# Kernel optimization log

Hardware: AMD Instinct MI355X
Metric: run time of the kernel (lower is better)

Reference implementation:

```python
import jax, jax.numpy as jnp
import numpy as np

B, S, I, H, O = 64, 512, 256, 1024, 128

def setup_inputs() -> dict:
    key = jax.random.key(0)
    ks = jax.random.split(key, 9)
    s_in = 1.0 / np.sqrt(I)
    s_h = 1.0 / np.sqrt(H)
    return {
        "x": jax.random.normal(ks[0], (B, S, I), dtype=jnp.float32),
        "W_in": jax.random.uniform(ks[1], (H, I), jnp.float32, -s_in, s_in),
        "b_in": jax.random.uniform(ks[2], (H,), jnp.float32, -s_in, s_in),
        "W_rec": jax.random.uniform(ks[3], (H, H), jnp.float32, -s_h, s_h),
        "b_rec": jax.random.uniform(ks[4], (H,), jnp.float32, -s_h, s_h),
        "tau_m": jnp.full((H,), 2.0, dtype=jnp.float32),
        "tau_n": jnp.full((H,), 2.0, dtype=jnp.float32),
        "W_out": jax.random.uniform(ks[5], (O, H), jnp.float32, -s_h, s_h),
        "b_out": jax.random.uniform(ks[6], (O,), jnp.float32, -s_h, s_h),
    }

def reference(x, W_in, b_in, W_rec, b_rec, tau_m, tau_n, W_out, b_out):
    b, s, _ = x.shape
    h = W_in.shape[0]
    alpha = jax.nn.sigmoid(tau_m)  # [H]
    beta = jax.nn.sigmoid(tau_n)   # [H]
    # Precompute feedforward GEMM for all timesteps at once: [B,S,H]
    ff = jnp.einsum('bsi,hi->bsh', x, W_in) + b_in

    def step(carry, ff_t):
        mem, d, prev_spike = carry  # each [B,H]
        total = ff_t + prev_spike @ W_rec.T + b_rec
        d = beta * d + (1.0 - beta) * total
        mem = alpha * mem + (1.0 - alpha) * d
        spike = (mem > 1.0).astype(mem.dtype)
        mem = mem * (1.0 - spike)
        out = jax.nn.sigmoid(spike @ W_out.T + b_out)  # [B,O]
        return (mem, d, spike), out

    zeros = jnp.zeros((b, h), dtype=x.dtype)
    _, outs = jax.lax.scan(step, (zeros, zeros, zeros), jnp.swapaxes(ff, 0, 1))
    return jnp.swapaxes(outs, 0, 1)  # [B,S,O]
```

## Files before the change

kernel.cpp:

```cpp
#include <hip/hip_runtime.h>
#include <hip/hip_bf16.h>
#include <stdint.h>

#define B_ 64
#define S_ 512
#define I_ 256
#define H_ 1024
#define O_ 128
#define M_ (B_*S_)

typedef float f32x4 __attribute__((ext_vector_type(4)));
typedef unsigned short u16x4 __attribute__((ext_vector_type(4)));
typedef unsigned short u16x8 __attribute__((ext_vector_type(8)));

__device__ __forceinline__ unsigned short f2bf(float f) {
    unsigned u = __float_as_uint(f);
    u += 0x7FFFu + ((u >> 16) & 1u);
    return (unsigned short)(u >> 16);
}
__device__ __forceinline__ float bf2f(unsigned short s) {
    return __uint_as_float((unsigned)s << 16);
}

__global__ void __launch_bounds__(256) k0_convert(
    const float* __restrict__ x, const float* __restrict__ Win,
    uint8_t* __restrict__ xf8, uint8_t* __restrict__ wf8,
    unsigned* __restrict__ firstCross)
{
    __shared__ unsigned lds32[64 * 65];
    const int i = blockIdx.x;
    const int t = threadIdx.x;

    const float* src;
    uint8_t* dstBase;
    int kqStride;
    if (i < 512) {
        const int r0 = i * 64;
        src = x + (size_t)r0 * 256;
        const int T = i >> 1;
        const int rbase = (i & 1) * 4;
        dstBase = xf8 + (size_t)T * 32768 + rbase * 512;
        kqStride = 4096;
    } else {
        const int i2 = i - 512;
        src = Win + (size_t)(i2 * 64) * 256;
        dstBase = wf8 + (size_t)i2 * 16384;
        kqStride = 2048;
    }

#pragma unroll
    for (int j = 0; j < 16; ++j) {
        const int f = j * 256 + t;
        const int lrow = f >> 6, c4 = f & 63;
        float4 v = *(const float4*)(src + (size_t)lrow * 256 + c4 * 4);
        int w0 = 0;
        w0 = __builtin_amdgcn_cvt_pk_fp8_f32(v.x, v.y, w0, false);
        w0 = __builtin_amdgcn_cvt_pk_fp8_f32(v.z, v.w, w0, true);
        lds32[lrow * 65 + c4] = (unsigned)w0;
    }
    __syncthreads();

#pragma unroll
    for (int j = 0; j < 4; ++j) {
        const int c = j * 256 + t;
        const int kq  = c >> 7;
        const int rem = c & 127;
        const int rbl = rem >> 5;
        const int l0  = (rem & 31) * 2;
        const int r   = l0 & 15;
        const int q   = l0 >> 4;
        const int lrow = rbl * 16 + r;
        const int c0 = kq * 8 + q * 2;
        uint4 o;
        o.x = lds32[lrow * 65 + c0];
        o.y = lds32[lrow * 65 + c0 + 1];
        o.z = lds32[(lrow + 1) * 65 + c0];
        o.w = lds32[(lrow + 1) * 65 + c0 + 1];
        *(uint4*)(dstBase + kq * kqStride + rbl * 512 + l0 * 8) = o;
    }

    if (i == 0 && t < 64) firstCross[t] = 0xFFFFFFFFu;
}

__global__ void __launch_bounds__(256, 4) kf_gemm_scan(
    const uint8_t* __restrict__ xf8, const uint8_t* __restrict__ wf8,
    const float* __restrict__ b_in, const float* __restrict__ b_rec,
    const float* __restrict__ tau_m, const float* __restrict__ tau_n,
    unsigned* __restrict__ firstCross)
{
    __shared__ uint8_t lsbuf[16384];

    const int tid  = threadIdx.x;
    const int w    = tid >> 6;
    const int lane = tid & 63;
    const int idx  = blockIdx.x;
    const int b    = (idx & 7) | ((idx >> 7) << 3);
    const int hn   = (idx >> 3) & 15;
    const int colrow = lane & 15;
    const int quad   = lane >> 4;

    float alpha = 0.f, beta = 0.f, cbr = 0.f, oma = 0.f, ombr = 0.f;
    float d = 0.f, mem = 0.f;
    unsigned cross = 0xFFFFFFFFu;
    if (tid < 64) {
        const int hs = hn * 64 + tid;
        alpha = 1.f / (1.f + expf(-tau_m[hs]));
        beta  = 1.f / (1.f + expf(-tau_n[hs]));
        oma = 1.f - alpha; ombr = 1.f - beta;
        cbr = ombr * (b_in[hs] + b_rec[hs]);
    }

    const uint8_t* wB = wf8 + (size_t)hn * 16384 + lane * 8;
    long long bq[32];
#pragma unroll
    for (int kq = 0; kq < 8; ++kq)
#pragma unroll
        for (int ni = 0; ni < 4; ++ni)
            bq[kq * 4 + ni] = *(const long long*)(wB + kq * 2048 + ni * 512);

    for (int tt = 0; tt < 4; ++tt) {
        const uint8_t* xA = xf8 + (size_t)(b * 4 + tt) * 32768
                          + w * 1024 + lane * 8;

        f32x4 acc[2][4];
#pragma unroll
        for (int mi = 0; mi < 2; ++mi)
#pragma unroll
            for (int ni = 0; ni < 4; ++ni)
                acc[mi][ni] = (f32x4){0.f, 0.f, 0.f, 0.f};

#pragma unroll
        for (int kq = 0; kq < 8; ++kq) {
            long long a[2];
#pragma unroll
            for (int mi = 0; mi < 2; ++mi)
                a[mi] = *(const long long*)(xA + kq * 4096 + mi * 512);
#pragma unroll
            for (int mi = 0; mi < 2; ++mi)
#pragma unroll
                for (int ni = 0; ni < 4; ++ni)
                    acc[mi][ni] = __builtin_amdgcn_mfma_f32_16x16x32_fp8_fp8(
                        a[mi], bq[kq * 4 + ni], acc[mi][ni], 0, 0, 0);
        }

        __syncthreads();

#pragma unroll
        for (int mi = 0; mi < 2; ++mi) {
            const int t0 = w * 32 + mi * 16 + quad * 4;
            const int gb = (t0 >> 3) * 1024 + (t0 & 7) * 2;
#pragma unroll
            for (int ni = 0; ni < 4; ++ni) {
                const int h0 = ni * 16 + colrow;
                u16x4 p;
                p[0] = f2bf(acc[mi][ni][0]);
                p[1] = f2bf(acc[mi][ni][1]);
                p[2] = f2bf(acc[mi][ni][2]);
                p[3] = f2bf(acc[mi][ni][3]);
                *(u16x4*)(lsbuf + gb + h0 * 16) = p;
            }
        }
        __syncthreads();

        if (tid < 64) {
            const uint8_t* rowp = lsbuf + tid * 16;
            for (int tl0 = 0; tl0 < 128; tl0 += 16) {
                const int gb = (tl0 >> 3) * 1024;
                u16x8 v0 = *(const u16x8*)(rowp + gb);
                u16x8 v1 = *(const u16x8*)(rowp + gb + 1024);
                float f[16];
#pragma unroll
                for (int u = 0; u < 8; ++u) { f[u] = bf2f(v0[u]); f[8 + u] = bf2f(v1[u]); }
#pragma unroll
                for (int u = 0; u < 16; ++u) {
                    d   = fmaf(beta,  d,   fmaf(ombr, f[u], cbr));
                    mem = fmaf(alpha, mem, oma * d);
                    if (mem > 1.0f) {
                        unsigned ts = (unsigned)(tt * 128 + tl0 + u);
                        if (ts < cross) cross = ts;
                    }
                }
            }
        }
    }

    if (tid < 64 && cross != 0xFFFFFFFFu) atomicMin(firstCross + b, cross);
}

__global__ void __launch_bounds__(1024) k3_repair(
    const float* __restrict__ x, const float* __restrict__ W_in,
    const float* __restrict__ b_in,
    const float* __restrict__ W_rec, const float* __restrict__ b_rec,
    const float* __restrict__ tau_m, const float* __restrict__ tau_n,
    const float* __restrict__ W_out, const float* __restrict__ b_out,
    const unsigned* __restrict__ firstCross,
    unsigned long long* __restrict__ gmask,
    float* __restrict__ out)
{
    const int b = blockIdx.x;
    if (firstCross[b] == 0xFFFFFFFFu) return;
    const int h = threadIdx.x;
    __shared__ float xrow[I_];
    __shared__ unsigned long long msk[16];
    if (h < 16) msk[h] = 0ull;
    const float alpha = 1.f / (1.f + expf(-tau_m[h]));
    const float beta  = 1.f / (1.f + expf(-tau_n[h]));
    const float bsum  = b_in[h] + b_rec[h];
    const float* wi = W_in + (size_t)h * I_;
    const float* wr = W_rec + (size_t)h * H_;
    float d = 0.f, mem = 0.f;
    for (int t = 0; t < S_; ++t) {
        __syncthreads();
        if (h < I_) xrow[h] = x[((size_t)b * S_ + t) * I_ + h];
        __syncthreads();
        float ffv = 0.f;
        for (int k = 0; k < I_; ++k) ffv += xrow[k] * wi[k];
        float rec = 0.f;
#pragma unroll
        for (int wd = 0; wd < 16; ++wd) {
            unsigned long long mw = msk[wd];
            while (mw) {
                int bit = __ffsll((long long)mw) - 1;
                rec += wr[(wd << 6) + bit];
                mw &= (mw - 1);
            }
        }
        float tot = ffv + bsum + rec;
        d   = beta  * d   + (1.f - beta)  * tot;
        mem = alpha * mem + (1.f - alpha) * d;
        int sp = (mem > 1.0f) ? 1 : 0;
        if (sp) mem = 0.f;
        unsigned long long bal = __ballot(sp);
        __syncthreads();
        if ((h & 63) == 0) {
            msk[h >> 6] = bal;
            gmask[((size_t)b * S_ + t) * 16 + (h >> 6)] = bal;
        }
    }
    __syncthreads();
    __threadfence_block();
    for (int i = h; i < S_ * O_; i += 1024) {
        const int t = i >> 7, o = i & (O_ - 1);
        float logit = b_out[o];
        const unsigned long long* m = gmask + ((size_t)b * S_ + t) * 16;
        const float* wo = W_out + (size_t)o * H_;
        for (int wd = 0; wd < 16; ++wd) {
            unsigned long long mw = m[wd];
            while (mw) {
                int bit = __ffsll((long long)mw) - 1;
                logit += wo[(wd << 6) + bit];
                mw &= (mw - 1);
            }
        }
        out[((size_t)b * S_ + t) * O_ + o] = 1.f / (1.f + expf(-logit));
    }
}

__global__ void __launch_bounds__(256) k4_out(
    const float* __restrict__ b_out,
    const unsigned* __restrict__ firstCross,
    float* __restrict__ out)
{
    const int i4 = blockIdx.x * 256 + threadIdx.x;
    const int b  = i4 >> 14;
    if (firstCross[b] != 0xFFFFFFFFu) return;
    const int o4 = i4 & 31;
    float4 v = *(const float4*)(b_out + o4 * 4);
    float4 r;
    r.x = 1.f / (1.f + expf(-v.x));
    r.y = 1.f / (1.f + expf(-v.y));
    r.z = 1.f / (1.f + expf(-v.z));
    r.w = 1.f / (1.f + expf(-v.w));
    *(float4*)(out + (size_t)i4 * 4) = r;
}

extern "C" void kernel_launch(void* const* d_in, const int* in_sizes, int n_in,
                              void* d_out, int out_size, void* d_ws, size_t ws_size,
                              hipStream_t stream) {
    const float* x     = (const float*)d_in[0];
    const float* W_in  = (const float*)d_in[1];
    const float* b_in  = (const float*)d_in[2];
    const float* W_rec = (const float*)d_in[3];
    const float* b_rec = (const float*)d_in[4];
    const float* tau_m = (const float*)d_in[5];
    const float* tau_n = (const float*)d_in[6];
    const float* W_out = (const float*)d_in[7];
    const float* b_out = (const float*)d_in[8];
    float* out = (float*)d_out;

    char* ws = (char*)d_ws;
    size_t off = 0;
    uint8_t* xf8 = (uint8_t*)(ws + off);               off += (size_t)M_ * I_;
    uint8_t* wf8 = (uint8_t*)(ws + off);               off += (size_t)H_ * I_;
    unsigned long long* gmask = (unsigned long long*)(ws + off); off += (size_t)B_ * S_ * 16 * 8;
    unsigned* firstCross = (unsigned*)(ws + off);      off += 256;
    if (ws_size < off) return;

    k0_convert<<<528, 256, 0, stream>>>(x, W_in, xf8, wf8, firstCross);
    kf_gemm_scan<<<1024, 256, 0, stream>>>(xf8, wf8, b_in, b_rec, tau_m, tau_n,
                                           firstCross);
    k3_repair<<<64, 1024, 0, stream>>>(x, W_in, b_in, W_rec, b_rec, tau_m, tau_n,
                                       W_out, b_out, firstCross, gmask, out);
    k4_out<<<4096, 256, 0, stream>>>(b_out, firstCross, out);
}
```

Baseline: 136.5 us.

## Warp-specialize GEMM-scan kernel with double-buffered LDS and halve convert block size

```diff
diff --git a/kernel.cpp b/kernel.cpp
--- a/kernel.cpp
+++ b/kernel.cpp
@@ -27,29 +27,26 @@
     uint8_t* __restrict__ xf8, uint8_t* __restrict__ wf8,
     unsigned* __restrict__ firstCross)
 {
-    __shared__ unsigned lds32[64 * 65];
+    __shared__ unsigned lds32[32 * 65];
     const int i = blockIdx.x;
     const int t = threadIdx.x;
 
     const float* src;
     uint8_t* dstBase;
     int kqStride;
-    if (i < 512) {
-        const int r0 = i * 64;
-        src = x + (size_t)r0 * 256;
-        const int T = i >> 1;
-        const int rbase = (i & 1) * 4;
-        dstBase = xf8 + (size_t)T * 32768 + rbase * 512;
+    if (i < 1024) {
+        src = x + (size_t)(i * 32) * 256;
+        dstBase = xf8 + (size_t)(i >> 2) * 32768 + (i & 3) * 2 * 512;
         kqStride = 4096;
     } else {
-        const int i2 = i - 512;
-        src = Win + (size_t)(i2 * 64) * 256;
-        dstBase = wf8 + (size_t)i2 * 16384;
+        const int i2 = i - 1024;
+        src = Win + (size_t)(i2 * 32) * 256;
+        dstBase = wf8 + (size_t)(i2 >> 1) * 16384 + (i2 & 1) * 2 * 512;
         kqStride = 2048;
     }
 
 #pragma unroll
-    for (int j = 0; j < 16; ++j) {
+    for (int j = 0; j < 8; ++j) {
         const int f = j * 256 + t;
         const int lrow = f >> 6, c4 = f & 63;
         float4 v = *(const float4*)(src + (size_t)lrow * 256 + c4 * 4);
@@ -61,12 +58,11 @@
     __syncthreads();
 
 #pragma unroll
-    for (int j = 0; j < 4; ++j) {
+    for (int j = 0; j < 2; ++j) {
         const int c = j * 256 + t;
-        const int kq  = c >> 7;
-        const int rem = c & 127;
-        const int rbl = rem >> 5;
-        const int l0  = (rem & 31) * 2;
+        const int kq  = c >> 6;
+        const int rbl = (c >> 5) & 1;
+        const int l0  = (c & 31) * 2;
         const int r   = l0 & 15;
         const int q   = l0 >> 4;
         const int lrow = rbl * 16 + r;
@@ -82,13 +78,14 @@
     if (i == 0 && t < 64) firstCross[t] = 0xFFFFFFFFu;
 }
 
-__global__ void __launch_bounds__(256, 4) kf_gemm_scan(
+__global__ void __launch_bounds__(320) kf_gemm_scan(
     const uint8_t* __restrict__ xf8, const uint8_t* __restrict__ wf8,
     const float* __restrict__ b_in, const float* __restrict__ b_rec,
     const float* __restrict__ tau_m, const float* __restrict__ tau_n,
     unsigned* __restrict__ firstCross)
 {
-    __shared__ uint8_t lsbuf[16384];
+    __shared__ uint8_t lB[16384];
+    __shared__ uint8_t lS[2][16384];
 
     const int tid  = threadIdx.x;
     const int w    = tid >> 6;
@@ -99,71 +96,76 @@
     const int colrow = lane & 15;
     const int quad   = lane >> 4;
 
+    if (w < 4) {
+        const uint8_t* gB = wf8 + (size_t)hn * 16384;
+#pragma unroll
+        for (int j = 0; j < 4; ++j) {
+            const int off = (w * 4 + j) * 1024 + lane * 16;
+            __builtin_amdgcn_global_load_lds(
+                (const __attribute__((address_space(1))) void*)(gB + off),
+                (__attribute__((address_space(3))) void*)(lB + off), 16, 0, 0);
+        }
+    }
+
     float alpha = 0.f, beta = 0.f, cbr = 0.f, oma = 0.f, ombr = 0.f;
     float d = 0.f, mem = 0.f;
     unsigned cross = 0xFFFFFFFFu;
-    if (tid < 64) {
-        const int hs = hn * 64 + tid;
+    if (w == 4) {
+        const int hs = hn * 64 + lane;
         alpha = 1.f / (1.f + expf(-tau_m[hs]));
         beta  = 1.f / (1.f + expf(-tau_n[hs]));
         oma = 1.f - alpha; ombr = 1.f - beta;
         cbr = ombr * (b_in[hs] + b_rec[hs]);
     }
-
-    const uint8_t* wB = wf8 + (size_t)hn * 16384 + lane * 8;
-    long long bq[32];
-#pragma unroll
-    for (int kq = 0; kq < 8; ++kq)
-#pragma unroll
-        for (int ni = 0; ni < 4; ++ni)
-            bq[kq * 4 + ni] = *(const long long*)(wB + kq * 2048 + ni * 512);
+    __syncthreads();
 
     for (int tt = 0; tt < 4; ++tt) {
-        const uint8_t* xA = xf8 + (size_t)(b * 4 + tt) * 32768
-                          + w * 1024 + lane * 8;
-
-        f32x4 acc[2][4];
-#pragma unroll
-        for (int mi = 0; mi < 2; ++mi)
-#pragma unroll
-            for (int ni = 0; ni < 4; ++ni)
-                acc[mi][ni] = (f32x4){0.f, 0.f, 0.f, 0.f};
-
-#pragma unroll
-        for (int kq = 0; kq < 8; ++kq) {
-            long long a[2];
+        if (w < 4) {
+            const uint8_t* xA = xf8 + (size_t)(b * 4 + tt) * 32768
+                              + w * 1024 + lane * 8;
+            long long a[16];
+#pragma unroll
+            for (int kq = 0; kq < 8; ++kq) {
+                a[kq * 2]     = *(const long long*)(xA + kq * 4096);
+                a[kq * 2 + 1] = *(const long long*)(xA + kq * 4096 + 512);
+            }
+            f32x4 acc[2][4];
 #pragma unroll
             for (int mi = 0; mi < 2; ++mi)
-                a[mi] = *(const long long*)(xA + kq * 4096 + mi * 512);
-#pragma unroll
-            for (int mi = 0; mi < 2; ++mi)
 #pragma unroll
                 for (int ni = 0; ni < 4; ++ni)
-                    acc[mi][ni] = __builtin_amdgcn_mfma_f32_16x16x32_fp8_fp8(
-                        a[mi], bq[kq * 4 + ni], acc[mi][ni], 0, 0, 0);
-        }
-
-        __syncthreads();
-
-#pragma unroll
-        for (int mi = 0; mi < 2; ++mi) {
-            const int t0 = w * 32 + mi * 16 + quad * 4;
-            const int gb = (t0 >> 3) * 1024 + (t0 & 7) * 2;
-#pragma unroll
-            for (int ni = 0; ni < 4; ++ni) {
-                const int h0 = ni * 16 + colrow;
-                u16x4 p;
-                p[0] = f2bf(acc[mi][ni][0]);
-                p[1] = f2bf(acc[mi][ni][1]);
-                p[2] = f2bf(acc[mi][ni][2]);
-                p[3] = f2bf(acc[mi][ni][3]);
-                *(u16x4*)(lsbuf + gb + h0 * 16) = p;
-            }
-        }
-        __syncthreads();
-
-        if (tid < 64) {
-            const uint8_t* rowp = lsbuf + tid * 16;
+                    acc[mi][ni] = (f32x4){0.f, 0.f, 0.f, 0.f};
+#pragma unroll
+            for (int kq = 0; kq < 8; ++kq) {
+                long long bfr[4];
+#pragma unroll
+                for (int ni = 0; ni < 4; ++ni)
+                    bfr[ni] = *(const long long*)(lB + kq * 2048 + ni * 512 + lane * 8);
+#pragma unroll
+                for (int mi = 0; mi < 2; ++mi)
+#pragma unroll
+                    for (int ni = 0; ni < 4; ++ni)
+                        acc[mi][ni] = __builtin_amdgcn_mfma_f32_16x16x32_fp8_fp8(
+                            a[kq * 2 + mi], bfr[ni], acc[mi][ni], 0, 0, 0);
+            }
+            uint8_t* buf = lS[tt & 1];
+#pragma unroll
+            for (int mi = 0; mi < 2; ++mi) {
+                const int t0 = w * 32 + mi * 16 + quad * 4;
+                const int gb = (t0 >> 3) * 1024 + (t0 & 7) * 2;
+#pragma unroll
+                for (int ni = 0; ni < 4; ++ni) {
+                    const int h0 = ni * 16 + colrow;
+                    u16x4 p;
+                    p[0] = f2bf(acc[mi][ni][0]);
+                    p[1] = f2bf(acc[mi][ni][1]);
+                    p[2] = f2bf(acc[mi][ni][2]);
+                    p[3] = f2bf(acc[mi][ni][3]);
+                    *(u16x4*)(buf + gb + h0 * 16) = p;
+                }
+            }
+        } else if (tt > 0) {
+            const uint8_t* rowp = lS[(tt - 1) & 1] + lane * 16;
             for (int tl0 = 0; tl0 < 128; tl0 += 16) {
                 const int gb = (tl0 >> 3) * 1024;
                 u16x8 v0 = *(const u16x8*)(rowp + gb);
@@ -176,15 +178,36 @@
                     d   = fmaf(beta,  d,   fmaf(ombr, f[u], cbr));
                     mem = fmaf(alpha, mem, oma * d);
                     if (mem > 1.0f) {
-                        unsigned ts = (unsigned)(tt * 128 + tl0 + u);
+                        unsigned ts = (unsigned)((tt - 1) * 128 + tl0 + u);
                         if (ts < cross) cross = ts;
                     }
                 }
             }
         }
-    }
-
-    if (tid < 64 && cross != 0xFFFFFFFFu) atomicMin(firstCross + b, cross);
+        __syncthreads();
+    }
+
+    if (w == 4) {
+        const uint8_t* rowp = lS[1] + lane * 16;
+        for (int tl0 = 0; tl0 < 128; tl0 += 16) {
+            const int gb = (tl0 >> 3) * 1024;
+            u16x8 v0 = *(const u16x8*)(rowp + gb);
+            u16x8 v1 = *(const u16x8*)(rowp + gb + 1024);
+            float f[16];
+#pragma unroll
+            for (int u = 0; u < 8; ++u) { f[u] = bf2f(v0[u]); f[8 + u] = bf2f(v1[u]); }
+#pragma unroll
+            for (int u = 0; u < 16; ++u) {
+                d   = fmaf(beta,  d,   fmaf(ombr, f[u], cbr));
+                mem = fmaf(alpha, mem, oma * d);
+                if (mem > 1.0f) {
+                    unsigned ts = (unsigned)(3 * 128 + tl0 + u);
+                    if (ts < cross) cross = ts;
+                }
+            }
+        }
+        if (cross != 0xFFFFFFFFu) atomicMin(firstCross + b, cross);
+    }
 }
 
 __global__ void __launch_bounds__(1024) k3_repair(
@@ -296,8 +319,8 @@
     unsigned* firstCross = (unsigned*)(ws + off);      off += 256;
     if (ws_size < off) return;
 
-    k0_convert<<<528, 256, 0, stream>>>(x, W_in, xf8, wf8, firstCross);
-    kf_gemm_scan<<<1024, 256, 0, stream>>>(xf8, wf8, b_in, b_rec, tau_m, tau_n,
+    k0_convert<<<1056, 256, 0, stream>>>(x, W_in, xf8, wf8, firstCross);
+    kf_gemm_scan<<<1024, 320, 0, stream>>>(xf8, wf8, b_in, b_rec, tau_m, tau_n,
                                            firstCross);
     k3_repair<<<64, 1024, 0, stream>>>(x, W_in, b_in, W_rec, b_rec, tau_m, tau_n,
                                        W_out, b_out, firstCross, gmask, out);
```

Result: slower. 144.6 us (+5.9%).
